# Kernel optimization log

Measured on AMD Instinct MI355X. Metric: run time of the kernel, lower is better.

## Reference

```python
import jax, jax.numpy as jnp
import numpy as np

UNITS = 3  # keras LSTM(units=3)


def lstm(x, W, U, b, return_sequences):
    """Keras-semantics LSTM. x: (B, T, D). Gate order i, f, g(c), o."""
    xz = jnp.einsum('btd,dg->btg', x, W) + b  # precompute input projection (B, T, 4U)
    B = x.shape[0]
    h0 = jnp.zeros((B, UNITS), x.dtype)
    c0 = jnp.zeros((B, UNITS), x.dtype)

    def step(carry, zt):
        h, c = carry
        z = zt + h @ U  # (B, 4U)
        i, f, g, o = jnp.split(z, 4, axis=-1)
        i = jax.nn.sigmoid(i)
        f = jax.nn.sigmoid(f)
        g = jnp.tanh(g)
        o = jax.nn.sigmoid(o)
        c = f * c + i * g
        h = o * jnp.tanh(c)
        return (h, c), h

    (hT, _), hs = jax.lax.scan(step, (h0, c0), jnp.swapaxes(xz, 0, 1))
    return jnp.swapaxes(hs, 0, 1) if return_sequences else hT


def setup_inputs() -> dict:
    key = jax.random.key(0)
    ks = jax.random.split(key, 16)
    B, T = 8192, 256
    inp = {"state": jax.random.normal(ks[0], (B, T), jnp.float32)}
    in_dims = [1, UNITS, UNITS, UNITS]
    for l in range(4):
        inp[f"w{l+1}"] = jax.random.normal(ks[1 + 3 * l], (in_dims[l], 4 * UNITS), jnp.float32) * 0.3
        inp[f"u{l+1}"] = jax.random.normal(ks[2 + 3 * l], (UNITS, 4 * UNITS), jnp.float32) * 0.3
        inp[f"b{l+1}"] = jnp.zeros((4 * UNITS,), jnp.float32)
    inp["wd"] = jax.random.normal(ks[13], (UNITS, 1), jnp.float32) * 0.3
    inp["bd"] = jnp.zeros((1,), jnp.float32)
    return inp


def reference(state, w1, u1, b1, w2, u2, b2, w3, u3, b3, w4, u4, b4, wd, bd):
    x = state[..., None]  # (B, T, 1) -- np.reshape in original
    x = lstm(x, w1, u1, b1, True)
    x = lstm(x, w2, u2, b2, True)
    x = lstm(x, w3, u3, b3, True)
    h = lstm(x, w4, u4, b4, False)  # (B, 3), return_sequences=False
    out = h @ wd + bd               # Dense(units=1) -> (B, 1)
    return jnp.squeeze(out, axis=-1)[None, :]  # (1, B)
```

## Files before the change

### kernel.cpp

```cpp
#include <hip/hip_runtime.h>


#if __has_builtin(__builtin_amdgcn_rcpf)
__device__ __forceinline__ float frcp(float x) { return __builtin_amdgcn_rcpf(x); }
#else
__device__ __forceinline__ float frcp(float x) { return 1.0f / x; }
#endif

#if __has_builtin(__builtin_amdgcn_exp2f)
__device__ __forceinline__ float fexp2(float x) { return __builtin_amdgcn_exp2f(x); }
#else
__device__ __forceinline__ float fexp2(float x) { return exp2f(x); }
#endif

#define LOG2E 1.44269504088896340736f

__device__ __forceinline__ float sigm_pre(float zp) { return frcp(1.0f + fexp2(zp)); }
__device__ __forceinline__ float tanh_pre(float zp) { return 1.0f - 2.0f * frcp(1.0f + fexp2(zp)); }
__device__ __forceinline__ float tanh_(float x) {
    return 1.0f - 2.0f * frcp(1.0f + fexp2((2.0f * LOG2E) * x));
}


template<int K>
__device__ __forceinline__ float bcast4(float v) {
#if __has_builtin(__builtin_amdgcn_mov_dpp)
    int i = __builtin_amdgcn_mov_dpp(__float_as_int(v), K * 0x55, 0xF, 0xF, true);
    return __int_as_float(i);
#else
    return __shfl(v, (int)((threadIdx.x & ~3u) | K), 64);
#endif
}

__device__ __forceinline__ float shr4(float v) {
#if __has_builtin(__builtin_amdgcn_mov_dpp)
    int i = __builtin_amdgcn_mov_dpp(__float_as_int(v), 0x114, 0xF, 0xF, true);
    return __int_as_float(i);
#else
    float r = __shfl(v, (int)(threadIdx.x & 15u) - 4, 16);
    return ((threadIdx.x & 15u) >= 4) ? r : 0.0f;
#endif
}

template<bool MASK>
__device__ __forceinline__ void step(int n, float xs, int q,
                                     const float (&W)[3][4], const float (&U)[3][4],
                                     const float (&Bv)[4],
                                     float (&h)[3], float (&xin)[3], float &c)
{
    const float x0 = (q == 0) ? xs : xin[0];
    float z[4];
#pragma unroll
    for (int g = 0; g < 4; ++g) {
        float zz = Bv[g];
        zz = fmaf(x0,     W[0][g], zz);
        zz = fmaf(xin[1], W[1][g], zz);
        zz = fmaf(xin[2], W[2][g], zz);
        zz = fmaf(h[0],   U[0][g], zz);
        zz = fmaf(h[1],   U[1][g], zz);
        zz = fmaf(h[2],   U[2][g], zz);
        z[g] = zz;
    }
    const float ig = sigm_pre(z[0]);
    const float fg = sigm_pre(z[1]);
    const float gg = tanh_pre(z[2]);
    const float og = sigm_pre(z[3]);
    float cn = fmaf(fg, c, ig * gg);
    float hn = og * tanh_(cn);
    if (MASK) {
        const bool v = (n >= q);
        cn = v ? cn : c;
        hn = v ? hn : 0.0f;
    }
    c = cn;
    const float hb0 = bcast4<0>(hn);
    const float hb1 = bcast4<1>(hn);
    const float hb2 = bcast4<2>(hn);
    h[0] = hb0; h[1] = hb1; h[2] = hb2;
    xin[0] = shr4(hb0);
    xin[1] = shr4(hb1);
    xin[2] = shr4(hb2);
}

__global__ __launch_bounds__(256) void lstm_pipe(
    const float* __restrict__ state,
    const float* __restrict__ w1, const float* __restrict__ u1, const float* __restrict__ b1,
    const float* __restrict__ w2, const float* __restrict__ u2, const float* __restrict__ b2,
    const float* __restrict__ w3, const float* __restrict__ u3, const float* __restrict__ b3,
    const float* __restrict__ w4, const float* __restrict__ u4, const float* __restrict__ b4,
    const float* __restrict__ wd, const float* __restrict__ bd,
    float* __restrict__ out, int B)
{
    const int tid = blockIdx.x * 256 + threadIdx.x;
    const int e = tid >> 4;
    if (e >= B) return;
    const int l16 = tid & 15;
    const int q = l16 >> 2;
    const int u = l16 & 3;
    const int uu = (u < 3) ? u : 2;

    const float* Wp = (q == 0) ? w1 : (q == 1) ? w2 : (q == 2) ? w3 : w4;
    const float* Up = (q == 0) ? u1 : (q == 1) ? u2 : (q == 2) ? u3 : u4;
    const float* Bp = (q == 0) ? b1 : (q == 1) ? b2 : (q == 2) ? b3 : b4;
    const int nx = (q == 0) ? 1 : 3;

    float W[3][4], U[3][4], Bv[4];
#pragma unroll
    for (int g = 0; g < 4; ++g) {
        const float sc = (g == 2) ? (2.0f * LOG2E) : (-LOG2E);
        const int col = g * 3 + uu;
        Bv[g] = Bp[col] * sc;
#pragma unroll
        for (int k = 0; k < 3; ++k) {
            W[k][g] = (k < nx) ? Wp[k * 12 + col] * sc : 0.0f;
            U[k][g] = Up[k * 12 + col] * sc;
        }
    }

    float h[3]   = {0.f, 0.f, 0.f};
    float xin[3] = {0.f, 0.f, 0.f};
    float c = 0.f;

    const float4* sp = reinterpret_cast<const float4*>(state + (size_t)e * 256);

    float4 w = sp[0];
    step<true >(0, w.x, q, W, U, Bv, h, xin, c);
    step<true >(1, w.y, q, W, U, Bv, h, xin, c);
    step<true >(2, w.z, q, W, U, Bv, h, xin, c);
    float4 wn = sp[1];
    step<false>(3, w.w, q, W, U, Bv, h, xin, c);
    w = wn;

    for (int g4 = 1; g4 < 63; ++g4) {
        wn = sp[g4 + 1];
        step<false>(0, w.x, q, W, U, Bv, h, xin, c);
        step<false>(0, w.y, q, W, U, Bv, h, xin, c);
        step<false>(0, w.z, q, W, U, Bv, h, xin, c);
        step<false>(0, w.w, q, W, U, Bv, h, xin, c);
        w = wn;
    }
    step<false>(0, w.x, q, W, U, Bv, h, xin, c);
    step<false>(0, w.y, q, W, U, Bv, h, xin, c);
    step<false>(0, w.z, q, W, U, Bv, h, xin, c);
    step<false>(0, w.w, q, W, U, Bv, h, xin, c);

    step<false>(0, 0.f, q, W, U, Bv, h, xin, c);
    step<false>(0, 0.f, q, W, U, Bv, h, xin, c);
    step<false>(0, 0.f, q, W, U, Bv, h, xin, c);

    if (l16 == 12) {
        out[e] = fmaf(h[0], wd[0], fmaf(h[1], wd[1], fmaf(h[2], wd[2], bd[0])));
    }
}

extern "C" void kernel_launch(void* const* d_in, const int* in_sizes, int n_in,
                              void* d_out, int out_size, void* d_ws, size_t ws_size,
                              hipStream_t stream) {
    const float* state = (const float*)d_in[0];
    const float* w1 = (const float*)d_in[1];
    const float* u1 = (const float*)d_in[2];
    const float* b1 = (const float*)d_in[3];
    const float* w2 = (const float*)d_in[4];
    const float* u2 = (const float*)d_in[5];
    const float* b2 = (const float*)d_in[6];
    const float* w3 = (const float*)d_in[7];
    const float* u3 = (const float*)d_in[8];
    const float* b3 = (const float*)d_in[9];
    const float* w4 = (const float*)d_in[10];
    const float* u4 = (const float*)d_in[11];
    const float* b4 = (const float*)d_in[12];
    const float* wd = (const float*)d_in[13];
    const float* bd = (const float*)d_in[14];
    float* out = (float*)d_out;

    const int B = in_sizes[0] / 256;
    const long long threads = (long long)B * 16;
    const int grid = (int)((threads + 255) / 256);
    lstm_pipe<<<grid, 256, 0, stream>>>(state, w1, u1, b1, w2, u2, b2,
                                        w3, u3, b3, w4, u4, b4, wd, bd, out, B);
}
```

Before: 142.4 us.

## Process two batch rows per lane group and merge LSTM gate reciprocals

Each 16-lane group now advances two independent batch elements in an interleaved step, giving the scheduler two independent dependency chains to hide transcendental and DPP latency, at the cost of half as many threads. The gate and cell math is also restructured algebraically so the sigmoid and tanh divisions fold into two reciprocals per step instead of five, with a clamp on the cell tanh exponent to avoid overflow. The block size drops to 128, and fewer total waves means less parallelism across the device. The merged-reciprocal form may change rounding and overflow behaviour for large gate pre-activations.

```diff
diff --git a/kernel.cpp b/kernel.cpp
--- a/kernel.cpp
+++ b/kernel.cpp
@@ -14,13 +14,7 @@
 #endif
 
 #define LOG2E 1.44269504088896340736f
-
-__device__ __forceinline__ float sigm_pre(float zp) { return frcp(1.0f + fexp2(zp)); }
-__device__ __forceinline__ float tanh_pre(float zp) { return 1.0f - 2.0f * frcp(1.0f + fexp2(zp)); }
-__device__ __forceinline__ float tanh_(float x) {
-    return 1.0f - 2.0f * frcp(1.0f + fexp2((2.0f * LOG2E) * x));
-}
-
+#define KTWO  (2.0f * LOG2E)
 
 template<int K>
 __device__ __forceinline__ float bcast4(float v) {
@@ -43,46 +37,60 @@
 }
 
 template<bool MASK>
-__device__ __forceinline__ void step(int n, float xs, int q,
-                                     const float (&W)[3][4], const float (&U)[3][4],
-                                     const float (&Bv)[4],
-                                     float (&h)[3], float (&xin)[3], float &c)
+__device__ __forceinline__ void step2(int n, float xa, float xb, int q,
+                                      const float (&W)[3][4], const float (&U)[3][4],
+                                      const float (&Bv)[4],
+                                      float (&h)[2][3], float (&xin)[2][3],
+                                      float (&c)[2])
 {
-    const float x0 = (q == 0) ? xs : xin[0];
-    float z[4];
+    float z[2][4];
 #pragma unroll
-    for (int g = 0; g < 4; ++g) {
-        float zz = Bv[g];
-        zz = fmaf(x0,     W[0][g], zz);
-        zz = fmaf(xin[1], W[1][g], zz);
-        zz = fmaf(xin[2], W[2][g], zz);
-        zz = fmaf(h[0],   U[0][g], zz);
-        zz = fmaf(h[1],   U[1][g], zz);
-        zz = fmaf(h[2],   U[2][g], zz);
-        z[g] = zz;
+    for (int k = 0; k < 2; ++k) {
+        const float xs = k ? xb : xa;
+        const float x0 = (q == 0) ? xs : xin[k][0];
+#pragma unroll
+        for (int g = 0; g < 4; ++g) {
+            float zz = Bv[g];
+            zz = fmaf(x0,        W[0][g], zz);
+            zz = fmaf(xin[k][1], W[1][g], zz);
+            zz = fmaf(xin[k][2], W[2][g], zz);
+            zz = fmaf(h[k][0],   U[0][g], zz);
+            zz = fmaf(h[k][1],   U[1][g], zz);
+            zz = fmaf(h[k][2],   U[2][g], zz);
+            z[k][g] = zz;
+        }
     }
-    const float ig = sigm_pre(z[0]);
-    const float fg = sigm_pre(z[1]);
-    const float gg = tanh_pre(z[2]);
-    const float og = sigm_pre(z[3]);
-    float cn = fmaf(fg, c, ig * gg);
-    float hn = og * tanh_(cn);
-    if (MASK) {
-        const bool v = (n >= q);
-        cn = v ? cn : c;
-        hn = v ? hn : 0.0f;
+#pragma unroll
+    for (int k = 0; k < 2; ++k) {
+        const float I = fexp2(z[k][0]);
+        const float F = fexp2(z[k][1]);
+        const float G = fexp2(z[k][2]);
+        const float O = fexp2(z[k][3]);
+        const float DI = 1.0f + I, DF = 1.0f + F, DG = 1.0f + G, DO = 1.0f + O;
+        const float PIG = DI * DG;
+        const float num = fmaf(c[k], PIG, (G - 1.0f) * DF);
+        float cn = num * frcp(PIG * DF);
+        float Carg = KTWO * cn;
+        Carg = fminf(Carg, 80.0f);
+        const float C = fexp2(Carg);
+        float hn = (C - 1.0f) * frcp(DO * (1.0f + C));
+        if (MASK) {
+            const bool v = (n >= q);
+            cn = v ? cn : c[k];
+            hn = v ? hn : 0.0f;
+        }
+        c[k] = cn;
+        const float hb0 = bcast4<0>(hn);
+        const float hb1 = bcast4<1>(hn);
+        const float hb2 = bcast4<2>(hn);
+        h[k][0] = hb0; h[k][1] = hb1; h[k][2] = hb2;
+        xin[k][0] = shr4(hb0);
+        xin[k][1] = shr4(hb1);
+        xin[k][2] = shr4(hb2);
     }
-    c = cn;
-    const float hb0 = bcast4<0>(hn);
-    const float hb1 = bcast4<1>(hn);
-    const float hb2 = bcast4<2>(hn);
-    h[0] = hb0; h[1] = hb1; h[2] = hb2;
-    xin[0] = shr4(hb0);
-    xin[1] = shr4(hb1);
-    xin[2] = shr4(hb2);
 }
 
-__global__ __launch_bounds__(256) void lstm_pipe(
+__global__ __launch_bounds__(128) void lstm_pipe2(
     const float* __restrict__ state,
     const float* __restrict__ w1, const float* __restrict__ u1, const float* __restrict__ b1,
     const float* __restrict__ w2, const float* __restrict__ u2, const float* __restrict__ b2,
@@ -91,9 +99,12 @@
     const float* __restrict__ wd, const float* __restrict__ bd,
     float* __restrict__ out, int B)
 {
-    const int tid = blockIdx.x * 256 + threadIdx.x;
-    const int e = tid >> 4;
-    if (e >= B) return;
+    const int tid = blockIdx.x * 128 + threadIdx.x;
+    const int p = tid >> 4;
+    if (p >= ((B + 1) >> 1)) return;
+    const int e0 = 2 * p;
+    const int e1 = e0 + 1;
+    const bool has1 = (e1 < B);
     const int l16 = tid & 15;
     const int q = l16 >> 2;
     const int u = l16 & 3;
@@ -117,39 +128,42 @@
         }
     }
 
-    float h[3]   = {0.f, 0.f, 0.f};
-    float xin[3] = {0.f, 0.f, 0.f};
-    float c = 0.f;
+    float h[2][3]   = {{0.f,0.f,0.f},{0.f,0.f,0.f}};
+    float xin[2][3] = {{0.f,0.f,0.f},{0.f,0.f,0.f}};
+    float c[2] = {0.f, 0.f};
 
-    const float4* sp = reinterpret_cast<const float4*>(state + (size_t)e * 256);
+    const float4* sp0 = reinterpret_cast<const float4*>(state + (size_t)e0 * 256);
+    const float4* sp1 = reinterpret_cast<const float4*>(state + (size_t)(has1 ? e1 : e0) * 256);
 
-    float4 w = sp[0];
-    step<true >(0, w.x, q, W, U, Bv, h, xin, c);
-    step<true >(1, w.y, q, W, U, Bv, h, xin, c);
-    step<true >(2, w.z, q, W, U, Bv, h, xin, c);
-    float4 wn = sp[1];
-    step<false>(3, w.w, q, W, U, Bv, h, xin, c);
-    w = wn;
+    float4 wa = sp0[0], wb = sp1[0];
+    step2<true >(0, wa.x, wb.x, q, W, U, Bv, h, xin, c);
+    step2<true >(1, wa.y, wb.y, q, W, U, Bv, h, xin, c);
+    step2<true >(2, wa.z, wb.z, q, W, U, Bv, h, xin, c);
+    float4 na = sp0[1], nb = sp1[1];
+    step2<false>(3, wa.w, wb.w, q, W, U, Bv, h, xin, c);
+    wa = na; wb = nb;
 
     for (int g4 = 1; g4 < 63; ++g4) {
-        wn = sp[g4 + 1];
-        step<false>(0, w.x, q, W, U, Bv, h, xin, c);
-        step<false>(0, w.y, q, W, U, Bv, h, xin, c);
-        step<false>(0, w.z, q, W, U, Bv, h, xin, c);
-        step<false>(0, w.w, q, W, U, Bv, h, xin, c);
-        w = wn;
+        na = sp0[g4 + 1]; nb = sp1[g4 + 1];
+        step2<false>(0, wa.x, wb.x, q, W, U, Bv, h, xin, c);
+        step2<false>(0, wa.y, wb.y, q, W, U, Bv, h, xin, c);
+        step2<false>(0, wa.z, wb.z, q, W, U, Bv, h, xin, c);
+        step2<false>(0, wa.w, wb.w, q, W, U, Bv, h, xin, c);
+        wa = na; wb = nb;
     }
-    step<false>(0, w.x, q, W, U, Bv, h, xin, c);
-    step<false>(0, w.y, q, W, U, Bv, h, xin, c);
-    step<false>(0, w.z, q, W, U, Bv, h, xin, c);
-    step<false>(0, w.w, q, W, U, Bv, h, xin, c);
+    step2<false>(0, wa.x, wb.x, q, W, U, Bv, h, xin, c);
+    step2<false>(0, wa.y, wb.y, q, W, U, Bv, h, xin, c);
+    step2<false>(0, wa.z, wb.z, q, W, U, Bv, h, xin, c);
+    step2<false>(0, wa.w, wb.w, q, W, U, Bv, h, xin, c);
 
-    step<false>(0, 0.f, q, W, U, Bv, h, xin, c);
-    step<false>(0, 0.f, q, W, U, Bv, h, xin, c);
-    step<false>(0, 0.f, q, W, U, Bv, h, xin, c);
+    step2<false>(0, 0.f, 0.f, q, W, U, Bv, h, xin, c);
+    step2<false>(0, 0.f, 0.f, q, W, U, Bv, h, xin, c);
+    step2<false>(0, 0.f, 0.f, q, W, U, Bv, h, xin, c);
 
     if (l16 == 12) {
-        out[e] = fmaf(h[0], wd[0], fmaf(h[1], wd[1], fmaf(h[2], wd[2], bd[0])));
+        out[e0] = fmaf(h[0][0], wd[0], fmaf(h[0][1], wd[1], fmaf(h[0][2], wd[2], bd[0])));
+        if (has1)
+            out[e1] = fmaf(h[1][0], wd[0], fmaf(h[1][1], wd[1], fmaf(h[1][2], wd[2], bd[0])));
     }
 }
 
@@ -174,8 +188,9 @@
     float* out = (float*)d_out;
 
     const int B = in_sizes[0] / 256;
-    const long long threads = (long long)B * 16;
-    const int grid = (int)((threads + 255) / 256);
-    lstm_pipe<<<grid, 256, 0, stream>>>(state, w1, u1, b1, w2, u2, b2,
-                                        w3, u3, b3, w4, u4, b4, wd, bd, out, B);
+    const int pairs = (B + 1) >> 1;
+    const long long threads = (long long)pairs * 16;
+    const int grid = (int)((threads + 127) / 128);
+    lstm_pipe2<<<grid, 128, 0, stream>>>(state, w1, u1, b1, w2, u2, b2,
+                                         w3, u3, b3, w4, u4, b4, wd, bd, out, B);
 }
```

Result: slower. 193.2 us (+35.7%).
